# Optimization experiments

Measured on AMD Instinct MI355X. Metric: run time of the kernel, lower is better.

The kernel has to match this reference:

```python
import itertools
import jax, jax.numpy as jnp
import numpy as np

B, RES = 256, 16
DIM, KEY_DIM, NUM_HEADS, ATTN_RATIO = 448, 32, 8, 4
SEQ = RES * RES
EXP_KEY_DIM = ATTN_RATIO * KEY_DIM          # 128
TOTAL_KEY = KEY_DIM * NUM_HEADS             # 256
TOTAL_EXP = EXP_KEY_DIM * NUM_HEADS         # 1024
QKV_DIM = TOTAL_EXP + 2 * TOTAL_KEY         # 1536
SCALE = KEY_DIM ** -0.5


def _build_bias_idxs():
    # Replicates the itertools.product loop from build()
    points = list(itertools.product(range(RES), range(RES)))
    offsets = {}
    idxs = []
    for p1 in points:
        for p2 in points:
            off = (abs(p1[0] - p2[0]), abs(p1[1] - p2[1]))
            if off not in offsets:
                offsets[off] = len(offsets)
            idxs.append(offsets[off])
    return np.asarray(idxs, dtype=np.int32).reshape(SEQ, SEQ), len(offsets)


def setup_inputs() -> dict:
    key = jax.random.key(0)
    ks = jax.random.split(key, 6)
    bias_idxs_np, n_off = _build_bias_idxs()
    std = 0.02
    return {
        "hidden_states": jax.random.normal(ks[0], (B, SEQ, DIM), dtype=jnp.float32),
        "qkv_w": jax.random.normal(ks[1], (DIM, QKV_DIM), dtype=jnp.float32) * std,
        "qkv_b": jnp.zeros((QKV_DIM,), dtype=jnp.float32),
        "proj_w": jax.random.normal(ks[2], (TOTAL_EXP, DIM), dtype=jnp.float32) * std,
        "proj_b": jnp.zeros((DIM,), dtype=jnp.float32),
        "attention_biases": jax.random.normal(ks[3], (NUM_HEADS, n_off), dtype=jnp.float32) * std,
        "attention_bias_idxs": jnp.asarray(bias_idxs_np),
    }


def reference(hidden_states, qkv_w, qkv_b, proj_w, proj_b, attention_biases, attention_bias_idxs):
    b, s, _ = hidden_states.shape
    qkv = hidden_states @ qkv_w + qkv_b                       # [B,S,1536]
    qkv = qkv.reshape(b, s, NUM_HEADS, KEY_DIM * 2 + EXP_KEY_DIM)
    q, k, v = jnp.split(qkv, [KEY_DIM, 2 * KEY_DIM], axis=3)  # [B,S,H,dk],[B,S,H,dk],[B,S,H,dv]
    scores = jnp.einsum("bqhd,bkhd->bhqk", q, k) * SCALE      # [B,H,S,S]
    bias = attention_biases[:, attention_bias_idxs]           # [H,S,S] gather
    probs = jax.nn.softmax(scores + bias[None], axis=-1)
    ctx = jnp.einsum("bhqk,bkhd->bqhd", probs, v)             # [B,S,H,dv]
    ctx = ctx.reshape(b, s, TOTAL_EXP)
    return ctx @ proj_w + proj_b
```

## Files before the change

kernel.cpp:

```cpp
#include <hip/hip_runtime.h>
#include <hip/hip_bf16.h>
#include <stdint.h>


typedef __attribute__((ext_vector_type(4))) float f32x4;
typedef __attribute__((ext_vector_type(8))) short short8;
typedef __attribute__((ext_vector_type(4))) unsigned short u16x4;
typedef __attribute__((ext_vector_type(2))) unsigned int u32x2;

#define DEVINL static __device__ __forceinline__

DEVINL unsigned short f2bf(float f) {
  unsigned u = __float_as_uint(f);
  return (unsigned short)((u + 0x7FFFu + ((u >> 16) & 1u)) >> 16);
}
DEVINL float bf2f(short s) {
  return __uint_as_float(((unsigned)(unsigned short)s) << 16);
}
DEVINL unsigned cvt_pk_bf16(float lo, float hi) {
  unsigned r;
  asm("v_cvt_pk_bf16_f32 %0, %1, %2" : "=v"(r) : "v"(lo), "v"(hi));
  return r;
}

DEVINL void gload_lds16(const void* g, void* l) {
  __builtin_amdgcn_global_load_lds((const __attribute__((address_space(1))) void*)g,
                                   (__attribute__((address_space(3))) void*)l,
                                   16, 0, 0);
}

#define SCALE 0.17677669529663687f
#define LOG2E 1.4426950408889634f

#define WS_XB     ((size_t)0)
#define WS_CTX    ((size_t)0)
#define WS_WQT    ((size_t)134217728)
#define WS_WPT    ((size_t)135593984)
#define WS_QW     ((size_t)136642560)
#define WS_KW     ((size_t)170196992)
#define WS_VT     ((size_t)203751424)
#define WS_QKVBP  ((size_t)342163456)

DEVINL int qkv_perm(int np, float* sc) {
  *sc = 1.0f;
  if (np < 512) {
    const int h = np >> 6, c = np & 63;
    if (c < 32) *sc = SCALE * LOG2E;
    return h * 192 + c;
  }
  const int h = (np - 512) >> 7, e = (np - 512) & 127;
  return h * 192 + 64 + e;
}


__global__ void k_convert_x(const float* __restrict__ x, short* __restrict__ xb) {
  const size_t i = (size_t)blockIdx.x * blockDim.x + threadIdx.x;
  const f32x4* src = (const f32x4*)x + i * 2;
  f32x4 a = src[0], b = src[1];
  short8 o;
#pragma unroll
  for (int t = 0; t < 4; ++t) o[t] = (short)f2bf(a[t]);
#pragma unroll
  for (int t = 0; t < 4; ++t) o[4 + t] = (short)f2bf(b[t]);
  ((short8*)xb)[i] = o;
}

__global__ void k_prep_qkvw(const float* __restrict__ w, short* __restrict__ out) {
  const int idx = blockIdx.x * blockDim.x + threadIdx.x;
  if (idx >= 1536 * 448) return;
  const int np = idx / 448, k = idx - np * 448;
  float sc;
  const int n = qkv_perm(np, &sc);
  out[idx] = (short)f2bf(w[(size_t)k * 1536 + n] * sc);
}

__global__ void k_prep_qkvb(const float* __restrict__ bsrc, float* __restrict__ bdst) {
  const int np = blockIdx.x * blockDim.x + threadIdx.x;
  if (np >= 1536) return;
  float sc;
  const int n = qkv_perm(np, &sc);
  bdst[np] = bsrc[n] * sc;
}

__global__ void k_transpose_bf16(const float* __restrict__ in, short* __restrict__ out,
                                 int K, int N, int total) {
  const int idx = blockIdx.x * blockDim.x + threadIdx.x;
  if (idx >= total) return;
  const int n = idx / K, k = idx - n * K;
  const float v = (n < N) ? in[(size_t)k * N + n] : 0.0f;
  out[idx] = (short)f2bf(v);
}


template <int KSTEPS, int LDA, int LDB, bool SWAP>
DEVINL void gemm128_pipe(const short* __restrict__ A, const short* __restrict__ B,
                         short* Asm, short* Bsm, int m0, int n0, int tid,
                         f32x4 acc[4][4]) {
  const int lane = tid & 63, wave = tid >> 6;
  const int l15 = lane & 15, g = lane >> 4;
  const int wm = wave >> 1, wn = wave & 1;
  const int r8 = lane >> 3;
  const int scol = (((lane & 7) ^ r8) << 3);
  const int wbase = wave * 32;

  const short* Ab = A + (size_t)(m0 + wbase + r8) * LDA + scol;
  const short* Bb = B + (size_t)(n0 + wbase + r8) * LDB + scol;

#pragma unroll
  for (int c = 0; c < 4; ++c) {
    gload_lds16(Ab + (size_t)(c * 8) * LDA, Asm + (wbase + c * 8) * 64);
    gload_lds16(Bb + (size_t)(c * 8) * LDB, Bsm + (wbase + c * 8) * 64);
  }
  __syncthreads();

  for (int ks = 0; ks < KSTEPS; ++ks) {
    const int cur = ks & 1, nxt = cur ^ 1;
    if (ks + 1 < KSTEPS) {
      const int k0 = (ks + 1) * 64;
#pragma unroll
      for (int c = 0; c < 4; ++c) {
        gload_lds16(Ab + (size_t)(c * 8) * LDA + k0, Asm + nxt * 8192 + (wbase + c * 8) * 64);
        gload_lds16(Bb + (size_t)(c * 8) * LDB + k0, Bsm + nxt * 8192 + (wbase + c * 8) * 64);
      }
    }
#pragma unroll
    for (int s = 0; s < 2; ++s) {
      const int rslot = (((s * 4 + g) ^ (l15 & 7)) << 3);
      short8 a[4], b[4];
#pragma unroll
      for (int i = 0; i < 4; ++i)
        a[i] = *(const short8*)(Asm + cur * 8192 + (wm * 64 + i * 16 + l15) * 64 + rslot);
#pragma unroll
      for (int j = 0; j < 4; ++j)
        b[j] = *(const short8*)(Bsm + cur * 8192 + (wn * 64 + j * 16 + l15) * 64 + rslot);
#pragma unroll
      for (int i = 0; i < 4; ++i)
#pragma unroll
        for (int j = 0; j < 4; ++j)
          acc[i][j] = SWAP
              ? __builtin_amdgcn_mfma_f32_16x16x32_bf16(b[j], a[i], acc[i][j], 0, 0, 0)
              : __builtin_amdgcn_mfma_f32_16x16x32_bf16(a[i], b[j], acc[i][j], 0, 0, 0);
    }
    __syncthreads();
  }
}


template <int KSTEPS, int LDA, int LDB>
DEVINL void gemm128_pipe3(const short* __restrict__ A, const short* __restrict__ B,
                          short* Asm , short* Bsm ,
                          int m0, int n0, int tid, f32x4 acc[4][4]) {
  const int lane = tid & 63, wave = tid >> 6;
  const int l15 = lane & 15, g = lane >> 4;
  const int wm = wave >> 1, wn = wave & 1;
  const int r8 = lane >> 3;
  const int scol = (((lane & 7) ^ r8) << 3);
  const int wbase = wave * 32;

  const short* Ab = A + (size_t)(m0 + wbase + r8) * LDA + scol;
  const short* Bb = B + (size_t)(n0 + wbase + r8) * LDB + scol;

  auto stageA = [&](int k) {
    short* dst = Asm + (k % 3) * 8192 + wbase * 64;
    const short* src = Ab + (size_t)k * 64;
#pragma unroll
    for (int c = 0; c < 4; ++c) gload_lds16(src + (size_t)(c * 8) * LDA, dst + c * 512);
  };
  auto stageB = [&](int k) {
    short* dst = Bsm + (k % 2) * 8192 + wbase * 64;
    const short* src = Bb + (size_t)k * 64;
#pragma unroll
    for (int c = 0; c < 4; ++c) gload_lds16(src + (size_t)(c * 8) * LDB, dst + c * 512);
  };
  auto compute = [&](int k) {
    const short* Ac = Asm + (k % 3) * 8192;
    const short* Bc = Bsm + (k % 2) * 8192;
#pragma unroll
    for (int s = 0; s < 2; ++s) {
      const int rslot = (((s * 4 + g) ^ (l15 & 7)) << 3);
      short8 a[4], b[4];
#pragma unroll
      for (int i = 0; i < 4; ++i)
        a[i] = *(const short8*)(Ac + (wm * 64 + i * 16 + l15) * 64 + rslot);
#pragma unroll
      for (int j = 0; j < 4; ++j)
        b[j] = *(const short8*)(Bc + (wn * 64 + j * 16 + l15) * 64 + rslot);
#pragma unroll
      for (int i = 0; i < 4; ++i)
#pragma unroll
        for (int j = 0; j < 4; ++j)
          acc[i][j] = __builtin_amdgcn_mfma_f32_16x16x32_bf16(a[i], b[j], acc[i][j], 0, 0, 0);
    }
  };

  stageB(0); stageA(0); stageA(1);
  asm volatile("s_waitcnt vmcnt(4)" ::: "memory");
  __builtin_amdgcn_s_barrier();
  __builtin_amdgcn_sched_barrier(0);

#pragma unroll
  for (int ks = 0; ks < KSTEPS - 2; ++ks) {
    stageB(ks + 1);
    stageA(ks + 2);
    asm volatile("s_waitcnt vmcnt(12)" ::: "memory");
    __builtin_amdgcn_s_barrier();
    __builtin_amdgcn_sched_barrier(0);
    compute(ks);
    __builtin_amdgcn_s_barrier();
  }
  stageB(KSTEPS - 1);
  asm volatile("s_waitcnt vmcnt(8)" ::: "memory");
  __builtin_amdgcn_s_barrier();
  __builtin_amdgcn_sched_barrier(0);
  compute(KSTEPS - 2);
  __builtin_amdgcn_s_barrier();
  asm volatile("s_waitcnt vmcnt(0)" ::: "memory");
  __builtin_amdgcn_s_barrier();
  __builtin_amdgcn_sched_barrier(0);
  compute(KSTEPS - 1);
}


union QkvSmem {
  struct { short a[2 * 8192]; short b[2 * 8192]; } ab;
  short tile[128 * 136];
};

__global__ __launch_bounds__(256) void k_qkv_gemm(
    const short* __restrict__ Xb, const short* __restrict__ Wt,
    const float* __restrict__ qkvbp,
    short* __restrict__ Qw, short* __restrict__ Kw, short* __restrict__ Vt) {
  __shared__ __align__(16) QkvSmem sm;
  const int tid = threadIdx.x;
  const int l = (blockIdx.x & 7) * 768 + (blockIdx.x >> 3);
  const int mt = l / 12, by = l - mt * 12;
  const int m0 = mt * 128, n0 = by * 128;

  const int lane = tid & 63, wave = tid >> 6;
  const int l15 = lane & 15, g = lane >> 4;
  const int wm = wave >> 1, wn = wave & 1;
  const int b0 = m0 >> 8, s0 = m0 & 255;

  f32x4 acc[4][4];
#pragma unroll
  for (int i = 0; i < 4; ++i)
#pragma unroll
    for (int j = 0; j < 4; ++j) acc[i][j] = (f32x4){0.f, 0.f, 0.f, 0.f};

  if (by >= 4) {
    gemm128_pipe<7, 448, 448, false>(Xb, Wt, sm.ab.a, sm.ab.b, m0, n0, tid, acc);
#pragma unroll
    for (int i = 0; i < 4; ++i) {
#pragma unroll
      for (int j = 0; j < 4; ++j) {
        const float bv = qkvbp[n0 + wn * 64 + j * 16 + l15];
        u16x4 pk;
#pragma unroll
        for (int r = 0; r < 4; ++r) pk[r] = f2bf(acc[i][j][r] + bv);
        *(u16x4*)&sm.tile[(wn * 64 + j * 16 + l15) * 136 + wm * 64 + i * 16 + g * 4] = pk;
      }
    }
    __syncthreads();
    const int bh = b0 * 8 + (by - 4);
#pragma unroll
    for (int p = 0; p < 8; ++p) {
      const int er = p * 16 + (tid >> 4);
      const int sc = (tid & 15) * 8;
      short8 v = *(const short8*)&sm.tile[er * 136 + sc];
      *(short8*)(Vt + (size_t)bh * 33792 + er * 264 + s0 + sc) = v;
    }
  } else {
    gemm128_pipe<7, 448, 448, true>(Xb, Wt, sm.ab.a, sm.ab.b, m0, n0, tid, acc);
#pragma unroll
    for (int i = 0; i < 4; ++i) {
      const int s = s0 + wm * 64 + i * 16 + l15;
#pragma unroll
      for (int j = 0; j < 4; ++j) {
        const int nbase = n0 + wn * 64 + j * 16 + g * 4;
        const f32x4 bv4 = *(const f32x4*)(qkvbp + nbase);
        u16x4 pk;
#pragma unroll
        for (int r = 0; r < 4; ++r) pk[r] = f2bf(acc[i][j][r] + bv4[r]);
        const int c = nbase & 63;
        const int bh = b0 * 8 + (by << 1) + (nbase >> 6 & 1);
        short* dst = (c < 32) ? (Qw + ((size_t)bh * 256 + s) * 32 + c)
                              : (Kw + ((size_t)bh * 256 + s) * 32 + (c - 32));
        *(u16x4*)dst = pk;
      }
    }
  }
}


__global__ __launch_bounds__(512, 4) void k_attn(
    const short* __restrict__ Qw, const short* __restrict__ Kw,
    const short* __restrict__ Vt, const float* __restrict__ attb, int n_off,
    short* __restrict__ CTX) {
  __shared__ short Ps[4][32 * 264];
  __shared__ float rinv[2][4][32];
  __shared__ float bias_sm[256];

  const int tid = threadIdx.x, lane = tid & 63, wave = tid >> 6;
  const int l15 = lane & 15, g = lane >> 4;
  const int bh = blockIdx.x;
  const int b = bh >> 3, h = bh & 7;

  if (tid < 256) bias_sm[tid] = attb[h * n_off + tid] * LOG2E;
  __syncthreads();

  int offc[4];
#pragma unroll
  for (int r = 0; r < 4; ++r) {
    const int d = g * 4 + r - l15;
    offc[r] = (d < 0) ? -d : d;
  }

  const short* Qb = Qw + (size_t)bh * 8192;
  const short* Kb = Kw + (size_t)bh * 8192;
  const short* Vb = Vt + (size_t)bh * 33792;
  const int e = wave * 16 + l15;

  for (int ph = 0; ph < 2; ++ph) {
    const int Q0 = ph * 128;

    short8 aq[4][2];
#pragma unroll
    for (int u = 0; u < 4; ++u)
#pragma unroll
      for (int i = 0; i < 2; ++i)
        aq[u][i] = *(const short8*)(Qb + (Q0 + u * 32 + i * 16 + l15) * 32 + g * 8);
    short8 bkk[2];
#pragma unroll
    for (int fj = 0; fj < 2; ++fj)
      bkk[fj] = *(const short8*)(Kb + (wave * 32 + fj * 16 + l15) * 32 + g * 8);
    short8 bvv[8];
#pragma unroll
    for (int ks = 0; ks < 8; ++ks)
      bvv[ks] = *(const short8*)(Vb + e * 264 + ks * 32 + g * 8);

#pragma unroll
    for (int fj = 0; fj < 2; ++fj) {
      const int kk0 = wave * 32 + fj * 16;
      const int kr = wave * 2 + fj;
#pragma unroll
      for (int u = 0; u < 4; ++u) {
#pragma unroll
        for (int i = 0; i < 2; ++i) {
          const int qr = ph * 8 + u * 2 + i;
          const int ab = ((qr > kr) ? qr - kr : kr - qr) << 4;
          f32x4 acc;
#pragma unroll
          for (int r = 0; r < 4; ++r) acc[r] = bias_sm[ab + offc[r]];
          acc = __builtin_amdgcn_mfma_f32_16x16x32_bf16(bkk[fj], aq[u][i], acc, 0, 0, 0);
          u32x2 pk;
          pk.x = cvt_pk_bf16(exp2f(acc[0]), exp2f(acc[1]));
          pk.y = cvt_pk_bf16(exp2f(acc[2]), exp2f(acc[3]));
          *(u32x2*)&Ps[u][(i * 16 + l15) * 264 + kk0 + g * 4] = pk;
        }
      }
    }
    __syncthreads();

    {
      const int r = tid >> 4, part = tid & 15;
#pragma unroll
      for (int u = 0; u < 4; ++u) {
        const short* rowp = &Ps[u][r * 264 + part * 16];
        short8 x0 = ((const short8*)rowp)[0];
        short8 x1 = ((const short8*)rowp)[1];
        float sum = 0.f;
#pragma unroll
        for (int t = 0; t < 8; ++t) sum += bf2f(x0[t]) + bf2f(x1[t]);
#pragma unroll
        for (int d = 1; d < 16; d <<= 1) sum += __shfl_xor(sum, d);
        if (part == 0) rinv[ph][u][r] = 1.0f / sum;
      }
    }

    f32x4 cacc[4][2];
#pragma unroll
    for (int u = 0; u < 4; ++u)
#pragma unroll
      for (int qt = 0; qt < 2; ++qt) cacc[u][qt] = (f32x4){0.f, 0.f, 0.f, 0.f};

#pragma unroll
    for (int ks = 0; ks < 8; ++ks) {
#pragma unroll
      for (int u = 0; u < 4; ++u)
#pragma unroll
        for (int qt = 0; qt < 2; ++qt) {
          const short8 ap = *(const short8*)&Ps[u][(qt * 16 + l15) * 264 + ks * 32 + g * 8];
          cacc[u][qt] = __builtin_amdgcn_mfma_f32_16x16x32_bf16(ap, bvv[ks], cacc[u][qt], 0, 0, 0);
        }
    }
    __syncthreads();

#pragma unroll
    for (int u = 0; u < 4; ++u)
#pragma unroll
      for (int qt = 0; qt < 2; ++qt) {
        const int qb = qt * 16 + g * 4;
        const size_t base = ((size_t)b * 256 + Q0 + u * 32 + qb) * 1024 + h * 128 + wave * 16 + l15;
#pragma unroll
        for (int r = 0; r < 4; r += 2) {
          const unsigned pw = cvt_pk_bf16(cacc[u][qt][r] * rinv[ph][u][qb + r],
                                          cacc[u][qt][r + 1] * rinv[ph][u][qb + r + 1]);
          CTX[base + (size_t)r * 1024] = (short)(pw & 0xffffu);
          CTX[base + (size_t)(r + 1) * 1024] = (short)(pw >> 16);
        }
      }
  }
}


__global__ __launch_bounds__(256) void k_proj_gemm(
    const short* __restrict__ CTX, const short* __restrict__ Wpt,
    const float* __restrict__ projb, float* __restrict__ out) {
  __shared__ __align__(16) short Asm[3 * 8192];
  __shared__ __align__(16) short Bsm[2 * 8192];
  const int tid = threadIdx.x;
  const int l = (blockIdx.x & 7) * 256 + (blockIdx.x >> 3);
  const int mt = l >> 2, nt = l & 3;
  const int m0 = mt * 128, n0 = nt * 128;
  f32x4 acc[4][4];
#pragma unroll
  for (int i = 0; i < 4; ++i)
#pragma unroll
    for (int j = 0; j < 4; ++j) acc[i][j] = (f32x4){0.f, 0.f, 0.f, 0.f};

  gemm128_pipe3<16, 1024, 1024>(CTX, Wpt, Asm, Bsm, m0, n0, tid, acc);

  const int lane = tid & 63, wave = tid >> 6;
  const int l15 = lane & 15, g = lane >> 4;
  const int wm = wave >> 1, wn = wave & 1;
#pragma unroll
  for (int i = 0; i < 4; ++i) {
    const int mb = m0 + wm * 64 + i * 16 + g * 4;
#pragma unroll
    for (int j = 0; j < 4; ++j) {
      const int n = n0 + wn * 64 + j * 16 + l15;
      if (n < 448) {
        const float bv = projb[n];
#pragma unroll
        for (int r = 0; r < 4; ++r)
          out[(size_t)(mb + r) * 448 + n] = acc[i][j][r] + bv;
      }
    }
  }
}


extern "C" void kernel_launch(void* const* d_in, const int* in_sizes, int n_in,
                              void* d_out, int out_size, void* d_ws, size_t ws_size,
                              hipStream_t stream) {
  const float* X      = (const float*)d_in[0];
  const float* qkv_w  = (const float*)d_in[1];
  const float* qkv_b  = (const float*)d_in[2];
  const float* proj_w = (const float*)d_in[3];
  const float* proj_b = (const float*)d_in[4];
  const float* att_b  = (const float*)d_in[5];
  const int n_off = in_sizes[5] / 8;

  char* ws = (char*)d_ws;
  short* Xb    = (short*)(ws + WS_XB);
  short* CTX   = (short*)(ws + WS_CTX);
  short* WQT   = (short*)(ws + WS_WQT);
  short* WPT   = (short*)(ws + WS_WPT);
  short* Qw    = (short*)(ws + WS_QW);
  short* Kw    = (short*)(ws + WS_KW);
  short* Vt    = (short*)(ws + WS_VT);
  float* QKVBP = (float*)(ws + WS_QKVBP);

  k_convert_x<<<14336, 256, 0, stream>>>(X, Xb);
  k_prep_qkvw<<<(1536 * 448 + 255) / 256, 256, 0, stream>>>(qkv_w, WQT);
  k_prep_qkvb<<<6, 256, 0, stream>>>(qkv_b, QKVBP);
  k_transpose_bf16<<<(512 * 1024 + 255) / 256, 256, 0, stream>>>(proj_w, WPT, 1024, 448, 512 * 1024);

  k_qkv_gemm<<<6144, 256, 0, stream>>>(Xb, WQT, QKVBP, Qw, Kw, Vt);
  k_attn<<<2048, 512, 0, stream>>>(Qw, Kw, Vt, att_b, n_off, CTX);
  k_proj_gemm<<<2048, 256, 0, stream>>>(CTX, WPT, proj_b, (float*)d_out);
}
```

Measured before the change: 358.2 us.

## Use triple-buffered pipelined GEMM for QKV projection and add MFMA priority hints

```diff
diff --git a/kernel.cpp b/kernel.cpp
--- a/kernel.cpp
+++ b/kernel.cpp
@@ -93,60 +93,6 @@
 
 
 template <int KSTEPS, int LDA, int LDB, bool SWAP>
-DEVINL void gemm128_pipe(const short* __restrict__ A, const short* __restrict__ B,
-                         short* Asm, short* Bsm, int m0, int n0, int tid,
-                         f32x4 acc[4][4]) {
-  const int lane = tid & 63, wave = tid >> 6;
-  const int l15 = lane & 15, g = lane >> 4;
-  const int wm = wave >> 1, wn = wave & 1;
-  const int r8 = lane >> 3;
-  const int scol = (((lane & 7) ^ r8) << 3);
-  const int wbase = wave * 32;
-
-  const short* Ab = A + (size_t)(m0 + wbase + r8) * LDA + scol;
-  const short* Bb = B + (size_t)(n0 + wbase + r8) * LDB + scol;
-
-#pragma unroll
-  for (int c = 0; c < 4; ++c) {
-    gload_lds16(Ab + (size_t)(c * 8) * LDA, Asm + (wbase + c * 8) * 64);
-    gload_lds16(Bb + (size_t)(c * 8) * LDB, Bsm + (wbase + c * 8) * 64);
-  }
-  __syncthreads();
-
-  for (int ks = 0; ks < KSTEPS; ++ks) {
-    const int cur = ks & 1, nxt = cur ^ 1;
-    if (ks + 1 < KSTEPS) {
-      const int k0 = (ks + 1) * 64;
-#pragma unroll
-      for (int c = 0; c < 4; ++c) {
-        gload_lds16(Ab + (size_t)(c * 8) * LDA + k0, Asm + nxt * 8192 + (wbase + c * 8) * 64);
-        gload_lds16(Bb + (size_t)(c * 8) * LDB + k0, Bsm + nxt * 8192 + (wbase + c * 8) * 64);
-      }
-    }
-#pragma unroll
-    for (int s = 0; s < 2; ++s) {
-      const int rslot = (((s * 4 + g) ^ (l15 & 7)) << 3);
-      short8 a[4], b[4];
-#pragma unroll
-      for (int i = 0; i < 4; ++i)
-        a[i] = *(const short8*)(Asm + cur * 8192 + (wm * 64 + i * 16 + l15) * 64 + rslot);
-#pragma unroll
-      for (int j = 0; j < 4; ++j)
-        b[j] = *(const short8*)(Bsm + cur * 8192 + (wn * 64 + j * 16 + l15) * 64 + rslot);
-#pragma unroll
-      for (int i = 0; i < 4; ++i)
-#pragma unroll
-        for (int j = 0; j < 4; ++j)
-          acc[i][j] = SWAP
-              ? __builtin_amdgcn_mfma_f32_16x16x32_bf16(b[j], a[i], acc[i][j], 0, 0, 0)
-              : __builtin_amdgcn_mfma_f32_16x16x32_bf16(a[i], b[j], acc[i][j], 0, 0, 0);
-    }
-    __syncthreads();
-  }
-}
-
-
-template <int KSTEPS, int LDA, int LDB>
 DEVINL void gemm128_pipe3(const short* __restrict__ A, const short* __restrict__ B,
                           short* Asm , short* Bsm ,
                           int m0, int n0, int tid, f32x4 acc[4][4]) {
@@ -185,18 +131,21 @@
 #pragma unroll
       for (int j = 0; j < 4; ++j)
         b[j] = *(const short8*)(Bc + (wn * 64 + j * 16 + l15) * 64 + rslot);
+      __builtin_amdgcn_s_setprio(1);
 #pragma unroll
       for (int i = 0; i < 4; ++i)
 #pragma unroll
         for (int j = 0; j < 4; ++j)
-          acc[i][j] = __builtin_amdgcn_mfma_f32_16x16x32_bf16(a[i], b[j], acc[i][j], 0, 0, 0);
+          acc[i][j] = SWAP
+              ? __builtin_amdgcn_mfma_f32_16x16x32_bf16(b[j], a[i], acc[i][j], 0, 0, 0)
+              : __builtin_amdgcn_mfma_f32_16x16x32_bf16(a[i], b[j], acc[i][j], 0, 0, 0);
+      __builtin_amdgcn_s_setprio(0);
     }
   };
 
   stageB(0); stageA(0); stageA(1);
   asm volatile("s_waitcnt vmcnt(4)" ::: "memory");
   __builtin_amdgcn_s_barrier();
-  __builtin_amdgcn_sched_barrier(0);
 
 #pragma unroll
   for (int ks = 0; ks < KSTEPS - 2; ++ks) {
@@ -204,25 +153,22 @@
     stageA(ks + 2);
     asm volatile("s_waitcnt vmcnt(12)" ::: "memory");
     __builtin_amdgcn_s_barrier();
-    __builtin_amdgcn_sched_barrier(0);
     compute(ks);
     __builtin_amdgcn_s_barrier();
   }
   stageB(KSTEPS - 1);
   asm volatile("s_waitcnt vmcnt(8)" ::: "memory");
   __builtin_amdgcn_s_barrier();
-  __builtin_amdgcn_sched_barrier(0);
   compute(KSTEPS - 2);
   __builtin_amdgcn_s_barrier();
   asm volatile("s_waitcnt vmcnt(0)" ::: "memory");
   __builtin_amdgcn_s_barrier();
-  __builtin_amdgcn_sched_barrier(0);
   compute(KSTEPS - 1);
 }
 
 
 union QkvSmem {
-  struct { short a[2 * 8192]; short b[2 * 8192]; } ab;
+  struct { short a[3 * 8192]; short b[2 * 8192]; } ab;
   short tile[128 * 136];
 };
 
@@ -248,7 +194,8 @@
     for (int j = 0; j < 4; ++j) acc[i][j] = (f32x4){0.f, 0.f, 0.f, 0.f};
 
   if (by >= 4) {
-    gemm128_pipe<7, 448, 448, false>(Xb, Wt, sm.ab.a, sm.ab.b, m0, n0, tid, acc);
+    gemm128_pipe3<7, 448, 448, false>(Xb, Wt, sm.ab.a, sm.ab.b, m0, n0, tid, acc);
+    __syncthreads();
 #pragma unroll
     for (int i = 0; i < 4; ++i) {
 #pragma unroll
@@ -270,7 +217,7 @@
       *(short8*)(Vt + (size_t)bh * 33792 + er * 264 + s0 + sc) = v;
     }
   } else {
-    gemm128_pipe<7, 448, 448, true>(Xb, Wt, sm.ab.a, sm.ab.b, m0, n0, tid, acc);
+    gemm128_pipe3<7, 448, 448, true>(Xb, Wt, sm.ab.a, sm.ab.b, m0, n0, tid, acc);
 #pragma unroll
     for (int i = 0; i < 4; ++i) {
       const int s = s0 + wm * 64 + i * 16 + l15;
@@ -428,7 +375,7 @@
 #pragma unroll
     for (int j = 0; j < 4; ++j) acc[i][j] = (f32x4){0.f, 0.f, 0.f, 0.f};
 
-  gemm128_pipe3<16, 1024, 1024>(CTX, Wpt, Asm, Bsm, m0, n0, tid, acc);
+  gemm128_pipe3<16, 1024, 1024, false>(CTX, Wpt, Asm, Bsm, m0, n0, tid, acc);
 
   const int lane = tid & 63, wave = tid >> 6;
   const int l15 = lane & 15, g = lane >> 4;
```

New measurement: 367.5 us. 2.6% more time.
